# Performance work log

Hardware: AMD Instinct MI355X
Metric: run time of the kernel (lower is better)

## Reference

```python
import jax, jax.numpy as jnp
import numpy as np

B, H, N, D = 2, 16, 2048, 64


def setup_inputs() -> dict:
    key = jax.random.key(0)
    kq, kk, kv = jax.random.split(key, 3)
    q = jax.random.normal(kq, (B, H, N, D), dtype=jnp.float32)
    k = jax.random.normal(kk, (B, H, N, D), dtype=jnp.float32)
    v = jax.random.normal(kv, (B, H, N, D), dtype=jnp.float32)
    return {"q": q, "k": k, "v": v}


def reference(q, k, v):
    b, h, n, d = q.shape
    # add_zero_kv: prepend an all-zero key/value along the sequence dim
    k = jnp.pad(k, ((0, 0), (0, 0), (1, 0), (0, 0)))  # [b,h,n+1,d]
    v = jnp.pad(v, ((0, 0), (0, 0), (1, 0), (0, 0)))
    kv_len = n + 1

    # l2_distance augmentation: q'.k' = 2 q.k - |q|^2 - |k|^2 = -|q - k|^2
    k_sq = jnp.sum(k * k, axis=-1, keepdims=True)
    k_aug = jnp.concatenate([k, -jnp.ones_like(k_sq), k_sq], axis=-1)  # [b,h,kv,d+2]
    q_sq = jnp.sum(q * q, axis=-1, keepdims=True)
    q_aug = jnp.concatenate([2.0 * q, q_sq, -jnp.ones_like(q_sq)], axis=-1)  # [b,h,n,d+2]

    # SDPA default scale uses the AUGMENTED head dim (d + 2)
    scale = (d + 2) ** -0.5
    scores = jnp.einsum('bhid,bhjd->bhij', q_aug, k_aug) * scale  # [b,h,n,kv]

    # causal mask folded into boolean mask because kv_len > q_len:
    # create_causal_mask(n, kv) = triu(ones, kv - n + 1) masked; allowed where j <= i + (kv - n)
    i = jnp.arange(n)[:, None]
    j = jnp.arange(kv_len)[None, :]
    allowed = j <= i + (kv_len - n)  # [n, kv]

    neg = jnp.asarray(-jnp.inf, dtype=scores.dtype)
    scores = jnp.where(allowed[None, None], scores, neg)
    attn = jax.nn.softmax(scores, axis=-1)
    out = jnp.einsum('bhij,bhjd->bhid', attn, v)  # [b,h,n,d]
    return out
```

## Files before the change

### kernel.cpp

```cpp
#include <hip/hip_runtime.h>


#define NQ 2048
#define DH 64
#define NT 32

typedef float f32x4 __attribute__((ext_vector_type(4)));
typedef __bf16 bf16x8 __attribute__((ext_vector_type(8)));
typedef unsigned short u16x8 __attribute__((ext_vector_type(8)));

union B8 { u16x8 u; bf16x8 b; };

__device__ __forceinline__ unsigned short f2b(float f) {
  unsigned int x = __builtin_bit_cast(unsigned int, f);
  unsigned int r = x + 0x7fffu + ((x >> 16) & 1u);
  return (unsigned short)(r >> 16);
}
__device__ __forceinline__ float b2f(unsigned short u) {
  unsigned int t = ((unsigned int)u) << 16;
  return __builtin_bit_cast(float, t);
}

__device__ __forceinline__ int kslot(int a) {
  return (a & 0x23) | ((a & 0x04) << 2) | ((a & 0x18) >> 1);
}

__device__ __forceinline__ void gl_lds16(const void* g, void* l) {
  __builtin_amdgcn_global_load_lds(
      (const __attribute__((address_space(1))) unsigned int*)g,
      (__attribute__((address_space(3))) unsigned int*)l, 16, 0, 0);
}

constexpr float QS = 0.3551784733906239f;
constexpr float BS = 0.17758923669531197f;

__global__ __launch_bounds__(256) void build_ws(
    const float* __restrict__ k, const float* __restrict__ v,
    unsigned short* __restrict__ wsK, unsigned short* __restrict__ wsV,
    float* __restrict__ wsB)
{
  const int bh = blockIdx.x;
  const int t  = blockIdx.y;
  const int tid  = threadIdx.x;
  const int wid  = tid >> 6;
  const int lane = tid & 63;
  const size_t bhN = (size_t)bh * NQ;
  const int tile64 = t * 64;
  const size_t tileId = (size_t)bh * NT + t;
  unsigned short* Kt = wsK + tileId * 4096;
  unsigned short* Vt = wsV + tileId * 4096;
  float*          Bt = wsB + tileId * 64;

  __shared__ float sTb[64];

#pragma unroll
  for (int i = 0; i < 4; i++) {
    int f  = i * 256 + tid;
    int kg = f >> 4, d4 = f & 15;
    int slot = kslot(kg);
    const float4* kp = (const float4*)(k + (bhN + tile64 + kg) * DH);
    float4 kk = kp[d4];
    unsigned short h0 = f2b(kk.x), h1 = f2b(kk.y), h2 = f2b(kk.z), h3 = f2b(kk.w);
    float a0 = b2f(h0), a1 = b2f(h1), a2 = b2f(h2), a3 = b2f(h3);
    float ss = a0*a0 + a1*a1 + a2*a2 + a3*a3;
    ss += __shfl_xor(ss, 1, 64);
    ss += __shfl_xor(ss, 2, 64);
    ss += __shfl_xor(ss, 4, 64);
    ss += __shfl_xor(ss, 8, 64);
    if (d4 == 0) {
      float tb = __builtin_amdgcn_exp2f(-BS * ss);
      Bt[slot] = tb;
      sTb[kg]  = tb;
    }
    unsigned int w0 = (unsigned int)h0 | ((unsigned int)h1 << 16);
    unsigned int w1 = (unsigned int)h2 | ((unsigned int)h3 << 16);
    int idx = slot * 64 + ((d4 * 4) ^ ((slot & 7) << 3));
    uint2 wv; wv.x = w0; wv.y = w1;
    *(uint2*)&Kt[idx] = wv;
  }
  __syncthreads();

#pragma unroll
  for (int jj = 0; jj < 4; jj++) {
    int kgb = jj * 16 + wid * 4;
    const float* vp = v + (bhN + tile64 + kgb) * DH + lane;
    float x0 = vp[0] * sTb[kgb + 0];
    float x1 = vp[DH] * sTb[kgb + 1];
    float x2 = vp[2 * DH] * sTb[kgb + 2];
    float x3 = vp[3 * DH] * sTb[kgb + 3];
    unsigned int w0 = (unsigned int)f2b(x0) | ((unsigned int)f2b(x1) << 16);
    unsigned int w1 = (unsigned int)f2b(x2) | ((unsigned int)f2b(x3) << 16);
    int idx = lane * 64 + (kgb ^ ((lane & 7) << 3));
    uint2 wv; wv.x = w0; wv.y = w1;
    *(uint2*)&Vt[idx] = wv;
  }
}

__global__ __launch_bounds__(256) void attend_l2_flash(
    const float* __restrict__ q,
    const unsigned short* __restrict__ wsK,
    const unsigned short* __restrict__ wsV,
    const float* __restrict__ wsB,
    float* __restrict__ out)
{
  const int bh   = blockIdx.x;
  const int qt   = (gridDim.y - 1) - blockIdx.y;
  const int qbase = qt * 64;
  const int tid  = threadIdx.x;
  const int wid  = tid >> 6;
  const int lane = tid & 63;
  const int g    = lane >> 4;
  const int qi   = lane & 15;
  const int qg   = qbase + wid * 16 + qi;
  const size_t bhN = (size_t)bh * NQ;

  __shared__ __align__(16) unsigned short sK[3][4096];
  __shared__ __align__(16) unsigned short sV[3][4096];

  const float* qrow = q + (bhN + qg) * DH;
  bf16x8 q8[2];
#pragma unroll
  for (int ks = 0; ks < 2; ks++) {
    B8 th;
#pragma unroll
    for (int j = 0; j < 8; j++)
      th.u[j] = f2b(qrow[ks * 32 + g * 8 + j] * QS);
    q8[ks] = th.b;
  }

  f32x4 oacc[4] = { {0,0,0,0}, {0,0,0,0}, {0,0,0,0}, {0,0,0,0} };
  f32x4 l4 = {0, 0, 0, 0};

  const int ntiles = qt + 1;
  const size_t tbase = (size_t)bh * NT;
  const float* TB = wsB + tbase * 64;

  auto LTB = [&](int t, f32x4* tb) {
    const float* p = TB + t * 64 + 4 * g;
#pragma unroll
    for (int c = 0; c < 4; c++) tb[c] = *(const f32x4*)(p + 16 * c);
  };
  auto STAGE = [&](unsigned short* bK, unsigned short* bV, int t) {
    const char* Kt = (const char*)(wsK + (tbase + t) * 4096);
    const char* Vt = (const char*)(wsV + (tbase + t) * 4096);
#pragma unroll
    for (int c = 0; c < 2; c++) {
      int boff = wid * 2048 + c * 1024;
      gl_lds16(Kt + boff + lane * 16, (char*)bK + boff);
      gl_lds16(Vt + boff + lane * 16, (char*)bV + boff);
    }
  };

  unsigned short *kA = sK[0], *kB = sK[1], *kC = sK[2];
  unsigned short *vA = sV[0], *vB = sV[1], *vC = sV[2];
  f32x4 tb_cur[4], tb_nxt[4];

  STAGE(kA, vA, 0);
  LTB(0, tb_cur);
  if (ntiles > 1) {
    STAGE(kB, vB, 1);
    asm volatile("s_waitcnt vmcnt(4)" ::: "memory");
  } else {
    asm volatile("s_waitcnt vmcnt(0)" ::: "memory");
  }
  __builtin_amdgcn_s_barrier();

  for (int t = 0; t < ntiles; t++) {
    const bool hasN1 = (t + 1 < ntiles);
    const bool hasN2 = (t + 2 < ntiles);
    if (hasN1) LTB(t + 1, tb_nxt);
    __builtin_amdgcn_sched_barrier(0);
    if (hasN2) STAGE(kC, vC, t + 2);
    __builtin_amdgcn_sched_barrier(0);

    f32x4 sc[4] = { {0,0,0,0}, {0,0,0,0}, {0,0,0,0}, {0,0,0,0} };
#pragma unroll
    for (int c = 0; c < 4; c++) {
#pragma unroll
      for (int ks = 0; ks < 2; ks++) {
        int idx = (16 * c + qi) * 64 + ((ks * 32 + g * 8) ^ ((qi & 7) << 3));
        bf16x8 ak = *(const bf16x8*)&kA[idx];
        sc[c] = __builtin_amdgcn_mfma_f32_16x16x32_bf16(ak, q8[ks], sc[c], 0, 0, 0);
      }
    }

    if (t == ntiles - 1) {
      const int tile64 = t * 64;
#pragma unroll
      for (int c = 0; c < 4; c++)
#pragma unroll
        for (int r = 0; r < 4; r++) {
          int key = tile64 + 32 * (c >> 1) + 8 * g + 4 * (c & 1) + r;
          if (key > qg) sc[c][r] = -1e30f;
        }
    }

#pragma unroll
    for (int c = 0; c < 4; c++) {
#pragma unroll
      for (int r = 0; r < 4; r++) sc[c][r] = __builtin_amdgcn_exp2f(sc[c][r]);
#pragma unroll
      for (int r = 0; r < 4; r++) l4[r] = __builtin_fmaf(sc[c][r], tb_cur[c][r], l4[r]);
    }

    B8 t0, t1;
#pragma unroll
    for (int j = 0; j < 8; j++) {
      t0.b[j] = (__bf16)sc[(j >> 2)][j & 3];
      t1.b[j] = (__bf16)sc[2 + (j >> 2)][j & 3];
    }

#pragma unroll
    for (int db = 0; db < 4; db++) {
#pragma unroll
      for (int ks = 0; ks < 2; ks++) {
        int idx = (db * 16 + qi) * 64 + ((ks * 32 + g * 8) ^ ((qi & 7) << 3));
        bf16x8 av = *(const bf16x8*)&vA[idx];
        oacc[db] = __builtin_amdgcn_mfma_f32_16x16x32_bf16(av, (ks ? t1.b : t0.b),
                                                           oacc[db], 0, 0, 0);
      }
    }

    if (hasN2) asm volatile("s_waitcnt vmcnt(4)" ::: "memory");
    else       asm volatile("s_waitcnt vmcnt(0)" ::: "memory");
    __builtin_amdgcn_s_barrier();

    unsigned short* tk = kA; kA = kB; kB = kC; kC = tk;
    unsigned short* tv = vA; vA = vB; vB = vC; vC = tv;
#pragma unroll
    for (int c = 0; c < 4; c++) tb_cur[c] = tb_nxt[c];
  }

  float lt = (l4[0] + l4[1]) + (l4[2] + l4[3]);
  lt += __shfl_xor(lt, 16, 64);
  lt += __shfl_xor(lt, 32, 64);
  float denom = lt + 1.0f;
  float inv = 1.0f / denom;
  float* op = out + (bhN + qg) * DH;
#pragma unroll
  for (int db = 0; db < 4; db++) {
    float4 o;
    o.x = oacc[db][0] * inv;
    o.y = oacc[db][1] * inv;
    o.z = oacc[db][2] * inv;
    o.w = oacc[db][3] * inv;
    *(float4*)(op + db * 16 + 4 * g) = o;
  }
}

extern "C" void kernel_launch(void* const* d_in, const int* in_sizes, int n_in,
                              void* d_out, int out_size, void* d_ws, size_t ws_size,
                              hipStream_t stream) {
  (void)in_sizes; (void)n_in; (void)out_size; (void)ws_size;
  const float* q = (const float*)d_in[0];
  const float* k = (const float*)d_in[1];
  const float* v = (const float*)d_in[2];
  float* out = (float*)d_out;

  char* ws = (char*)d_ws;
  unsigned short* wsK = (unsigned short*)ws;
  unsigned short* wsV = (unsigned short*)(ws + (8u << 20));
  float*          wsB = (float*)(ws + (16u << 20));

  build_ws<<<dim3(32, NT), dim3(256), 0, stream>>>(k, v, wsK, wsV, wsB);
  attend_l2_flash<<<dim3(32, NT), dim3(256), 0, stream>>>(q, wsK, wsV, wsB, out);
}
```

Baseline: 49.15 us.

## Load V fragments directly from global in MFMA order, drop V LDS staging

The workspace builder now writes V tiles in the exact per-lane MFMA operand order, staged through shared memory. The attention kernel loads each lane's V fragments and row-bias values straight from global into registers each iteration instead of copying V into LDS. K keeps its triple-buffered LDS staging, now issued by all threads, with a clamped tile index so the wait counts stay uniform. This halves LDS use and removes V LDS reads, in exchange for redundant per-wave global reads of V and global load latency sitting before the PV MFMAs.

```diff
diff --git a/kernel.cpp b/kernel.cpp
--- a/kernel.cpp
+++ b/kernel.cpp
@@ -44,14 +44,17 @@
   const int tid  = threadIdx.x;
   const int wid  = tid >> 6;
   const int lane = tid & 63;
+  const int g    = lane >> 4;
+  const int qi   = lane & 15;
   const size_t bhN = (size_t)bh * NQ;
   const int tile64 = t * 64;
   const size_t tileId = (size_t)bh * NT + t;
-  unsigned short* Kt = wsK + tileId * 4096;
-  unsigned short* Vt = wsV + tileId * 4096;
-  float*          Bt = wsB + tileId * 64;
+  unsigned short* Kt  = wsK + tileId * 4096;
+  unsigned short* VtF = wsV + tileId * 4096;
+  float*          Bt  = wsB + tileId * 64;
 
   __shared__ float sTb[64];
+  __shared__ __align__(16) unsigned short sV[4096];
 
 #pragma unroll
   for (int i = 0; i < 4; i++) {
@@ -92,7 +95,17 @@
     unsigned int w1 = (unsigned int)f2b(x2) | ((unsigned int)f2b(x3) << 16);
     int idx = lane * 64 + (kgb ^ ((lane & 7) << 3));
     uint2 wv; wv.x = w0; wv.y = w1;
-    *(uint2*)&Vt[idx] = wv;
+    *(uint2*)&sV[idx] = wv;
+  }
+  __syncthreads();
+
+#pragma unroll
+  for (int f4 = 0; f4 < 2; f4++) {
+    int f  = wid * 2 + f4;
+    int cc = f >> 1, ks = f & 1;
+    int sw = ((ks * 32 + g * 8) ^ ((qi & 7) << 3));
+    bf16x8 vv = *(const bf16x8*)&sV[(cc * 16 + qi) * 64 + sw];
+    *(bf16x8*)&VtF[(f * 64 + lane) * 8] = vv;
   }
 }
 
@@ -115,7 +128,6 @@
   const size_t bhN = (size_t)bh * NQ;
 
   __shared__ __align__(16) unsigned short sK[3][4096];
-  __shared__ __align__(16) unsigned short sV[3][4096];
 
   const float* qrow = q + (bhN + qg) * DH;
   bf16x8 q8[2];
@@ -133,44 +145,40 @@
 
   const int ntiles = qt + 1;
   const size_t tbase = (size_t)bh * NT;
-  const float* TB = wsB + tbase * 64;
-
-  auto LTB = [&](int t, f32x4* tb) {
-    const float* p = TB + t * 64 + 4 * g;
-#pragma unroll
-    for (int c = 0; c < 4; c++) tb[c] = *(const f32x4*)(p + 16 * c);
+  const char*  Vws = (const char*)(wsV + tbase * 4096);
+  const float* TB  = wsB + tbase * 64;
+
+  auto STAGE_K = [&](unsigned short* bK, int t) {
+    const char* Kt = (const char*)(wsK + (tbase + t) * 4096);
+#pragma unroll
+    for (int c = 0; c < 2; c++)
+      gl_lds16(Kt + c * 4096 + tid * 16, (char*)bK + c * 4096 + tid * 16);
   };
-  auto STAGE = [&](unsigned short* bK, unsigned short* bV, int t) {
-    const char* Kt = (const char*)(wsK + (tbase + t) * 4096);
-    const char* Vt = (const char*)(wsV + (tbase + t) * 4096);
-#pragma unroll
-    for (int c = 0; c < 2; c++) {
-      int boff = wid * 2048 + c * 1024;
-      gl_lds16(Kt + boff + lane * 16, (char*)bK + boff);
-      gl_lds16(Vt + boff + lane * 16, (char*)bV + boff);
-    }
-  };
 
   unsigned short *kA = sK[0], *kB = sK[1], *kC = sK[2];
-  unsigned short *vA = sV[0], *vB = sV[1], *vC = sV[2];
-  f32x4 tb_cur[4], tb_nxt[4];
-
-  STAGE(kA, vA, 0);
-  LTB(0, tb_cur);
-  if (ntiles > 1) {
-    STAGE(kB, vB, 1);
-    asm volatile("s_waitcnt vmcnt(4)" ::: "memory");
-  } else {
-    asm volatile("s_waitcnt vmcnt(0)" ::: "memory");
-  }
+
+  STAGE_K(kA, 0);
+  __builtin_amdgcn_sched_barrier(0);
+  STAGE_K(kB, (ntiles > 1) ? 1 : 0);
+  __builtin_amdgcn_sched_barrier(0);
+  asm volatile("s_waitcnt vmcnt(2)" ::: "memory");
   __builtin_amdgcn_s_barrier();
 
   for (int t = 0; t < ntiles; t++) {
-    const bool hasN1 = (t + 1 < ntiles);
-    const bool hasN2 = (t + 2 < ntiles);
-    if (hasN1) LTB(t + 1, tb_nxt);
-    __builtin_amdgcn_sched_barrier(0);
-    if (hasN2) STAGE(kC, vC, t + 2);
+    const char* Vt = Vws + (size_t)t * 8192;
+    bf16x8 vf[8];
+#pragma unroll
+    for (int f = 0; f < 8; f++)
+      vf[f] = *(const bf16x8*)(Vt + f * 1024 + lane * 16);
+    __builtin_amdgcn_sched_barrier(0);
+
+    const float* bp = TB + t * 64 + 4 * g;
+    f32x4 tb[4];
+#pragma unroll
+    for (int c = 0; c < 4; c++) tb[c] = *(const f32x4*)(bp + 16 * c);
+    __builtin_amdgcn_sched_barrier(0);
+
+    STAGE_K(kC, (t + 2 < ntiles) ? (t + 2) : (ntiles - 1));
     __builtin_amdgcn_sched_barrier(0);
 
     f32x4 sc[4] = { {0,0,0,0}, {0,0,0,0}, {0,0,0,0}, {0,0,0,0} };
@@ -183,6 +191,10 @@
         sc[c] = __builtin_amdgcn_mfma_f32_16x16x32_bf16(ak, q8[ks], sc[c], 0, 0, 0);
       }
     }
+    __builtin_amdgcn_sched_barrier(0);
+
+    asm volatile("s_waitcnt vmcnt(2)" ::: "memory");
+    __builtin_amdgcn_sched_barrier(0);
 
     if (t == ntiles - 1) {
       const int tile64 = t * 64;
@@ -200,7 +212,7 @@
 #pragma unroll
       for (int r = 0; r < 4; r++) sc[c][r] = __builtin_amdgcn_exp2f(sc[c][r]);
 #pragma unroll
-      for (int r = 0; r < 4; r++) l4[r] = __builtin_fmaf(sc[c][r], tb_cur[c][r], l4[r]);
+      for (int r = 0; r < 4; r++) l4[r] = __builtin_fmaf(sc[c][r], tb[c][r], l4[r]);
     }
 
     B8 t0, t1;
@@ -214,21 +226,14 @@
     for (int db = 0; db < 4; db++) {
 #pragma unroll
       for (int ks = 0; ks < 2; ks++) {
-        int idx = (db * 16 + qi) * 64 + ((ks * 32 + g * 8) ^ ((qi & 7) << 3));
-        bf16x8 av = *(const bf16x8*)&vA[idx];
-        oacc[db] = __builtin_amdgcn_mfma_f32_16x16x32_bf16(av, (ks ? t1.b : t0.b),
+        oacc[db] = __builtin_amdgcn_mfma_f32_16x16x32_bf16(vf[db * 2 + ks],
+                                                           (ks ? t1.b : t0.b),
                                                            oacc[db], 0, 0, 0);
       }
     }
 
-    if (hasN2) asm volatile("s_waitcnt vmcnt(4)" ::: "memory");
-    else       asm volatile("s_waitcnt vmcnt(0)" ::: "memory");
     __builtin_amdgcn_s_barrier();
-
     unsigned short* tk = kA; kA = kB; kB = kC; kC = tk;
-    unsigned short* tv = vA; vA = vB; vB = vC; vC = tv;
-#pragma unroll
-    for (int c = 0; c < 4; c++) tb_cur[c] = tb_nxt[c];
   }
 
   float lt = (l4[0] + l4[1]) + (l4[2] + l4[3]);
```

After: 53.38 us. +8.6%, slower.

## Stage V one tile ahead with double buffer and interleave query-tile block order

Applied to the files above, without the earlier changes.

V now uses a double buffer and is loaded only one tile ahead, while K keeps a triple buffer loaded two tiles ahead. This cuts LDS from six to five tile buffers, which may allow more resident blocks per CU. Loads are issued unconditionally, with tile indices clamped at the end, so one fixed vmcnt(2) wait replaces the branchy waits, at the cost of some redundant tail loads. The grid becomes 1D, and blocks are remapped so short and long causal query tiles interleave instead of running longest-first, which may help or hurt tail load balance.

```diff
diff --git a/kernel.cpp b/kernel.cpp
--- a/kernel.cpp
+++ b/kernel.cpp
@@ -103,9 +103,14 @@
     const float* __restrict__ wsB,
     float* __restrict__ out)
 {
-  const int bh   = blockIdx.x;
-  const int qt   = (gridDim.y - 1) - blockIdx.y;
+  const int b    = blockIdx.x;
+  const int bh   = b & 31;
+  const int y    = b >> 5;
+  const int g5   = y & 7;
+  const int s    = y >> 3;
+  const int qt   = (s == 0) ? g5 : (s == 1) ? (31 - g5) : (s == 2) ? (8 + g5) : (23 - g5);
   const int qbase = qt * 64;
+
   const int tid  = threadIdx.x;
   const int wid  = tid >> 6;
   const int lane = tid & 63;
@@ -115,7 +120,7 @@
   const size_t bhN = (size_t)bh * NQ;
 
   __shared__ __align__(16) unsigned short sK[3][4096];
-  __shared__ __align__(16) unsigned short sV[3][4096];
+  __shared__ __align__(16) unsigned short sV[2][4096];
 
   const float* qrow = q + (bhN + qg) * DH;
   bf16x8 q8[2];
@@ -140,37 +145,43 @@
 #pragma unroll
     for (int c = 0; c < 4; c++) tb[c] = *(const f32x4*)(p + 16 * c);
   };
-  auto STAGE = [&](unsigned short* bK, unsigned short* bV, int t) {
+  auto STAGE_K = [&](unsigned short* bK, int t) {
     const char* Kt = (const char*)(wsK + (tbase + t) * 4096);
+#pragma unroll
+    for (int c = 0; c < 2; c++)
+      gl_lds16(Kt + c * 4096 + tid * 16, (char*)bK + c * 4096 + tid * 16);
+  };
+  auto STAGE_V = [&](unsigned short* bV, int t) {
     const char* Vt = (const char*)(wsV + (tbase + t) * 4096);
 #pragma unroll
-    for (int c = 0; c < 2; c++) {
-      int boff = wid * 2048 + c * 1024;
-      gl_lds16(Kt + boff + lane * 16, (char*)bK + boff);
-      gl_lds16(Vt + boff + lane * 16, (char*)bV + boff);
-    }
+    for (int c = 0; c < 2; c++)
+      gl_lds16(Vt + c * 4096 + tid * 16, (char*)bV + c * 4096 + tid * 16);
   };
 
   unsigned short *kA = sK[0], *kB = sK[1], *kC = sK[2];
-  unsigned short *vA = sV[0], *vB = sV[1], *vC = sV[2];
+  unsigned short *vA = sV[0], *vB = sV[1];
   f32x4 tb_cur[4], tb_nxt[4];
 
-  STAGE(kA, vA, 0);
+  STAGE_K(kA, 0);
+  __builtin_amdgcn_sched_barrier(0);
+  STAGE_V(vA, 0);
+  __builtin_amdgcn_sched_barrier(0);
   LTB(0, tb_cur);
-  if (ntiles > 1) {
-    STAGE(kB, vB, 1);
-    asm volatile("s_waitcnt vmcnt(4)" ::: "memory");
-  } else {
-    asm volatile("s_waitcnt vmcnt(0)" ::: "memory");
-  }
+  __builtin_amdgcn_sched_barrier(0);
+  STAGE_K(kB, (ntiles > 1) ? 1 : 0);
+  __builtin_amdgcn_sched_barrier(0);
+  asm volatile("s_waitcnt vmcnt(2)" ::: "memory");
   __builtin_amdgcn_s_barrier();
 
   for (int t = 0; t < ntiles; t++) {
-    const bool hasN1 = (t + 1 < ntiles);
-    const bool hasN2 = (t + 2 < ntiles);
-    if (hasN1) LTB(t + 1, tb_nxt);
+    const int t1 = (t + 1 < ntiles) ? (t + 1) : (ntiles - 1);
+    const int t2 = (t + 2 < ntiles) ? (t + 2) : (ntiles - 1);
+
+    LTB(t1, tb_nxt);
     __builtin_amdgcn_sched_barrier(0);
-    if (hasN2) STAGE(kC, vC, t + 2);
+    STAGE_V(vB, t1);
+    __builtin_amdgcn_sched_barrier(0);
+    STAGE_K(kC, t2);
     __builtin_amdgcn_sched_barrier(0);
 
     f32x4 sc[4] = { {0,0,0,0}, {0,0,0,0}, {0,0,0,0}, {0,0,0,0} };
@@ -203,11 +214,11 @@
       for (int r = 0; r < 4; r++) l4[r] = __builtin_fmaf(sc[c][r], tb_cur[c][r], l4[r]);
     }
 
-    B8 t0, t1;
+    B8 t0, t1r;
 #pragma unroll
     for (int j = 0; j < 8; j++) {
-      t0.b[j] = (__bf16)sc[(j >> 2)][j & 3];
-      t1.b[j] = (__bf16)sc[2 + (j >> 2)][j & 3];
+      t0.b[j]  = (__bf16)sc[(j >> 2)][j & 3];
+      t1r.b[j] = (__bf16)sc[2 + (j >> 2)][j & 3];
     }
 
 #pragma unroll
@@ -216,17 +227,16 @@
       for (int ks = 0; ks < 2; ks++) {
         int idx = (db * 16 + qi) * 64 + ((ks * 32 + g * 8) ^ ((qi & 7) << 3));
         bf16x8 av = *(const bf16x8*)&vA[idx];
-        oacc[db] = __builtin_amdgcn_mfma_f32_16x16x32_bf16(av, (ks ? t1.b : t0.b),
+        oacc[db] = __builtin_amdgcn_mfma_f32_16x16x32_bf16(av, (ks ? t1r.b : t0.b),
                                                            oacc[db], 0, 0, 0);
       }
     }
 
-    if (hasN2) asm volatile("s_waitcnt vmcnt(4)" ::: "memory");
-    else       asm volatile("s_waitcnt vmcnt(0)" ::: "memory");
+    asm volatile("s_waitcnt vmcnt(2)" ::: "memory");
     __builtin_amdgcn_s_barrier();
 
     unsigned short* tk = kA; kA = kB; kB = kC; kC = tk;
-    unsigned short* tv = vA; vA = vB; vB = vC; vC = tv;
+    unsigned short* tv = vA; vA = vB; vB = tv;
 #pragma unroll
     for (int c = 0; c < 4; c++) tb_cur[c] = tb_nxt[c];
   }
@@ -263,5 +273,5 @@
   float*          wsB = (float*)(ws + (16u << 20));
 
   build_ws<<<dim3(32, NT), dim3(256), 0, stream>>>(k, v, wsK, wsV, wsB);
-  attend_l2_flash<<<dim3(32, NT), dim3(256), 0, stream>>>(q, wsK, wsV, wsB, out);
-}
+  attend_l2_flash<<<dim3(1024), dim3(256), 0, stream>>>(q, wsK, wsV, wsB, out);
+}
```

Result: slower. 56.95 us (+15.9%).

## Process 128 query rows per block, reusing each K/V tile across two query fragments

Applied to the files above, without the earlier changes.

Each workgroup now handles a 128-row query tile: every wave owns two 16-row fragments that share the K and V tile loads from LDS. This halves K/V staging traffic and LDS reads per query and gives the MFMA pipe two independent chains to interleave. The grid is reordered to a 1D launch of 512 blocks, heaviest causal tiles first, and the staging addressing is simplified. In exchange each block does more work, the block count is halved so occupancy and load balance change, and register pressure roughly doubles for the accumulators.

```diff
diff --git a/kernel.cpp b/kernel.cpp
--- a/kernel.cpp
+++ b/kernel.cpp
@@ -103,35 +103,41 @@
     const float* __restrict__ wsB,
     float* __restrict__ out)
 {
-  const int bh   = blockIdx.x;
-  const int qt   = (gridDim.y - 1) - blockIdx.y;
-  const int qbase = qt * 64;
+  const int b    = blockIdx.x;
+  const int bh   = b & 31;
+  const int y    = b >> 5;
+  const int qt2  = (y < 8) ? (15 - y) : (y - 8);
+  const int ntiles = 2 * qt2 + 2;
+
   const int tid  = threadIdx.x;
   const int wid  = tid >> 6;
   const int lane = tid & 63;
   const int g    = lane >> 4;
   const int qi   = lane & 15;
-  const int qg   = qbase + wid * 16 + qi;
+  const int qg0  = qt2 * 128 + wid * 32 + qi;
+  const int qg1  = qg0 + 16;
   const size_t bhN = (size_t)bh * NQ;
 
   __shared__ __align__(16) unsigned short sK[3][4096];
   __shared__ __align__(16) unsigned short sV[3][4096];
 
-  const float* qrow = q + (bhN + qg) * DH;
-  bf16x8 q8[2];
-#pragma unroll
-  for (int ks = 0; ks < 2; ks++) {
-    B8 th;
-#pragma unroll
-    for (int j = 0; j < 8; j++)
-      th.u[j] = f2b(qrow[ks * 32 + g * 8 + j] * QS);
-    q8[ks] = th.b;
-  }
-
-  f32x4 oacc[4] = { {0,0,0,0}, {0,0,0,0}, {0,0,0,0}, {0,0,0,0} };
-  f32x4 l4 = {0, 0, 0, 0};
-
-  const int ntiles = qt + 1;
+  bf16x8 q8[2][2];
+#pragma unroll
+  for (int qf = 0; qf < 2; qf++) {
+    const float* qrow = q + (bhN + (qf ? qg1 : qg0)) * DH;
+#pragma unroll
+    for (int ks = 0; ks < 2; ks++) {
+      B8 th;
+#pragma unroll
+      for (int j = 0; j < 8; j++)
+        th.u[j] = f2b(qrow[ks * 32 + g * 8 + j] * QS);
+      q8[qf][ks] = th.b;
+    }
+  }
+
+  f32x4 oacc[2][4] = {};
+  f32x4 l4[2] = {{0,0,0,0},{0,0,0,0}};
+
   const size_t tbase = (size_t)bh * NT;
   const float* TB = wsB + tbase * 64;
 
@@ -145,9 +151,8 @@
     const char* Vt = (const char*)(wsV + (tbase + t) * 4096);
 #pragma unroll
     for (int c = 0; c < 2; c++) {
-      int boff = wid * 2048 + c * 1024;
-      gl_lds16(Kt + boff + lane * 16, (char*)bK + boff);
-      gl_lds16(Vt + boff + lane * 16, (char*)bV + boff);
+      gl_lds16(Kt + c * 4096 + tid * 16, (char*)bK + c * 4096 + tid * 16);
+      gl_lds16(Vt + c * 4096 + tid * 16, (char*)bV + c * 4096 + tid * 16);
     }
   };
 
@@ -156,13 +161,12 @@
   f32x4 tb_cur[4], tb_nxt[4];
 
   STAGE(kA, vA, 0);
+  __builtin_amdgcn_sched_barrier(0);
   LTB(0, tb_cur);
-  if (ntiles > 1) {
-    STAGE(kB, vB, 1);
-    asm volatile("s_waitcnt vmcnt(4)" ::: "memory");
-  } else {
-    asm volatile("s_waitcnt vmcnt(0)" ::: "memory");
-  }
+  __builtin_amdgcn_sched_barrier(0);
+  STAGE(kB, vB, 1);
+  __builtin_amdgcn_sched_barrier(0);
+  asm volatile("s_waitcnt vmcnt(4)" ::: "memory");
   __builtin_amdgcn_s_barrier();
 
   for (int t = 0; t < ntiles; t++) {
@@ -173,42 +177,52 @@
     if (hasN2) STAGE(kC, vC, t + 2);
     __builtin_amdgcn_sched_barrier(0);
 
-    f32x4 sc[4] = { {0,0,0,0}, {0,0,0,0}, {0,0,0,0}, {0,0,0,0} };
+    f32x4 sc[2][4] = {};
 #pragma unroll
     for (int c = 0; c < 4; c++) {
 #pragma unroll
       for (int ks = 0; ks < 2; ks++) {
         int idx = (16 * c + qi) * 64 + ((ks * 32 + g * 8) ^ ((qi & 7) << 3));
         bf16x8 ak = *(const bf16x8*)&kA[idx];
-        sc[c] = __builtin_amdgcn_mfma_f32_16x16x32_bf16(ak, q8[ks], sc[c], 0, 0, 0);
-      }
-    }
-
-    if (t == ntiles - 1) {
+        sc[0][c] = __builtin_amdgcn_mfma_f32_16x16x32_bf16(ak, q8[0][ks], sc[0][c], 0, 0, 0);
+        sc[1][c] = __builtin_amdgcn_mfma_f32_16x16x32_bf16(ak, q8[1][ks], sc[1][c], 0, 0, 0);
+      }
+    }
+
+    if (t >= ntiles - 2) {
       const int tile64 = t * 64;
 #pragma unroll
       for (int c = 0; c < 4; c++)
 #pragma unroll
         for (int r = 0; r < 4; r++) {
           int key = tile64 + 32 * (c >> 1) + 8 * g + 4 * (c & 1) + r;
-          if (key > qg) sc[c][r] = -1e30f;
+          if (key > qg0) sc[0][c][r] = -1e30f;
+          if (key > qg1) sc[1][c][r] = -1e30f;
         }
     }
 
 #pragma unroll
     for (int c = 0; c < 4; c++) {
 #pragma unroll
-      for (int r = 0; r < 4; r++) sc[c][r] = __builtin_amdgcn_exp2f(sc[c][r]);
-#pragma unroll
-      for (int r = 0; r < 4; r++) l4[r] = __builtin_fmaf(sc[c][r], tb_cur[c][r], l4[r]);
-    }
-
-    B8 t0, t1;
-#pragma unroll
-    for (int j = 0; j < 8; j++) {
-      t0.b[j] = (__bf16)sc[(j >> 2)][j & 3];
-      t1.b[j] = (__bf16)sc[2 + (j >> 2)][j & 3];
-    }
+      for (int r = 0; r < 4; r++) {
+        sc[0][c][r] = __builtin_amdgcn_exp2f(sc[0][c][r]);
+        sc[1][c][r] = __builtin_amdgcn_exp2f(sc[1][c][r]);
+      }
+#pragma unroll
+      for (int r = 0; r < 4; r++) {
+        l4[0][r] = __builtin_fmaf(sc[0][c][r], tb_cur[c][r], l4[0][r]);
+        l4[1][r] = __builtin_fmaf(sc[1][c][r], tb_cur[c][r], l4[1][r]);
+      }
+    }
+
+    B8 pr[2][2];
+#pragma unroll
+    for (int qf = 0; qf < 2; qf++)
+#pragma unroll
+      for (int j = 0; j < 8; j++) {
+        pr[qf][0].b[j] = (__bf16)sc[qf][(j >> 2)][j & 3];
+        pr[qf][1].b[j] = (__bf16)sc[qf][2 + (j >> 2)][j & 3];
+      }
 
 #pragma unroll
     for (int db = 0; db < 4; db++) {
@@ -216,8 +230,8 @@
       for (int ks = 0; ks < 2; ks++) {
         int idx = (db * 16 + qi) * 64 + ((ks * 32 + g * 8) ^ ((qi & 7) << 3));
         bf16x8 av = *(const bf16x8*)&vA[idx];
-        oacc[db] = __builtin_amdgcn_mfma_f32_16x16x32_bf16(av, (ks ? t1.b : t0.b),
-                                                           oacc[db], 0, 0, 0);
+        oacc[0][db] = __builtin_amdgcn_mfma_f32_16x16x32_bf16(av, pr[0][ks].b, oacc[0][db], 0, 0, 0);
+        oacc[1][db] = __builtin_amdgcn_mfma_f32_16x16x32_bf16(av, pr[1][ks].b, oacc[1][db], 0, 0, 0);
       }
     }
 
@@ -231,20 +245,23 @@
     for (int c = 0; c < 4; c++) tb_cur[c] = tb_nxt[c];
   }
 
-  float lt = (l4[0] + l4[1]) + (l4[2] + l4[3]);
-  lt += __shfl_xor(lt, 16, 64);
-  lt += __shfl_xor(lt, 32, 64);
-  float denom = lt + 1.0f;
-  float inv = 1.0f / denom;
-  float* op = out + (bhN + qg) * DH;
-#pragma unroll
-  for (int db = 0; db < 4; db++) {
-    float4 o;
-    o.x = oacc[db][0] * inv;
-    o.y = oacc[db][1] * inv;
-    o.z = oacc[db][2] * inv;
-    o.w = oacc[db][3] * inv;
-    *(float4*)(op + db * 16 + 4 * g) = o;
+#pragma unroll
+  for (int qf = 0; qf < 2; qf++) {
+    float lt = (l4[qf][0] + l4[qf][1]) + (l4[qf][2] + l4[qf][3]);
+    lt += __shfl_xor(lt, 16, 64);
+    lt += __shfl_xor(lt, 32, 64);
+    float denom = lt + 1.0f;
+    float inv = 1.0f / denom;
+    float* op = out + (bhN + (qf ? qg1 : qg0)) * DH;
+#pragma unroll
+    for (int db = 0; db < 4; db++) {
+      float4 o;
+      o.x = oacc[qf][db][0] * inv;
+      o.y = oacc[qf][db][1] * inv;
+      o.z = oacc[qf][db][2] * inv;
+      o.w = oacc[qf][db][3] * inv;
+      *(float4*)(op + db * 16 + 4 * g) = o;
+    }
   }
 }
 
@@ -263,5 +280,5 @@
   float*          wsB = (float*)(ws + (16u << 20));
 
   build_ws<<<dim3(32, NT), dim3(256), 0, stream>>>(k, v, wsK, wsV, wsB);
-  attend_l2_flash<<<dim3(32, NT), dim3(256), 0, stream>>>(q, wsK, wsV, wsB, out);
-}
+  attend_l2_flash<<<dim3(512), dim3(256), 0, stream>>>(q, wsK, wsV, wsB, out);
+}
```

Result: slower. 56.51 us (+15.0%).
